# Optimization experiments

Hardware: AMD Instinct MI355X
Metric: run time of the kernel (lower is better)

Reference implementation:

```python
import jax, jax.numpy as jnp
import numpy as np

N, E, IN_DIM, HID, OUT = 50000, 800000, 128, 128, 64


def setup_inputs() -> dict:
    key = jax.random.key(0)
    k = jax.random.split(key, 6)
    h = jax.random.normal(k[0], (N, IN_DIM), dtype=jnp.float32)
    edge_index = jax.random.randint(k[1], (2, E), 0, N, dtype=jnp.int64)
    s_in, s_hid = 1.0 / np.sqrt(IN_DIM), 1.0 / np.sqrt(HID)
    W_gcn = jax.random.uniform(k[2], (IN_DIM, HID), jnp.float32, -s_in, s_in)
    b_gcn = jnp.zeros((HID,), jnp.float32)
    W_fc = jax.random.uniform(k[3], (HID, OUT), jnp.float32, -s_hid, s_hid)
    b_fc = jax.random.uniform(k[4], (OUT,), jnp.float32, -s_hid, s_hid)
    return {"h": h, "edge_index": edge_index, "W_gcn": W_gcn,
            "b_gcn": b_gcn, "W_fc": W_fc, "b_fc": b_fc}


def reference(h, edge_index, W_gcn, b_gcn, W_fc, b_fc):
    n = h.shape[0]
    # GCNConv: transform, add self-loops, symmetric normalization, scatter-add
    x = h @ W_gcn                                   # [N, HID]
    loop = jnp.arange(n, dtype=edge_index.dtype)
    row = jnp.concatenate([edge_index[0], loop])    # source nodes
    col = jnp.concatenate([edge_index[1], loop])    # destination nodes
    deg = jax.ops.segment_sum(jnp.ones_like(col, dtype=x.dtype), col,
                              num_segments=n)       # in-degree incl. self-loop
    dinv = jnp.where(deg > 0, jax.lax.rsqrt(deg), 0.0)
    norm = dinv[row] * dinv[col]                    # [E+N]
    msg = x[row] * norm[:, None]                    # gather + scale
    agg = jax.ops.segment_sum(msg, col, num_segments=n) + b_gcn
    # ReLU then projection
    return jax.nn.relu(agg) @ W_fc + b_fc
```

## Files before the change

kernel.cpp:

```cpp
#include <hip/hip_runtime.h>

#define N_NODES 50000
#define N_EDGES 800000
#define NBKT 196
#define BINB 196
#define CASTB 391
#define BCAP 6144
#define SECAP 1792
#define UTS 136

typedef __attribute__((ext_vector_type(4))) float floatx4;
typedef __attribute__((ext_vector_type(8))) _Float16 half8;
typedef __attribute__((ext_vector_type(4))) _Float16 half4;
typedef __attribute__((ext_vector_type(2))) _Float16 half2v;

#define O_GF    0UL
#define O_DEG   3200UL
#define O_W1    203264UL
#define O_W2    236032UL
#define O_STG   252416UL
#define O_H16   5857792UL

__global__ __launch_bounds__(256) void k_bin(const int* __restrict__ ei,
                                             const float* __restrict__ h,
                                             int* __restrict__ gfill,
                                             unsigned* __restrict__ staging,
                                             const float* __restrict__ Wg,
                                             const float* __restrict__ Wf,
                                             _Float16* __restrict__ W1,
                                             _Float16* __restrict__ W2,
                                             _Float16* __restrict__ h16) {
    int b = blockIdx.x, t = threadIdx.x;
    if (b >= BINB + 96) {
        int wb = b - (BINB + 96);
        int nb = wb * 128;
        int nn = min(128, N_NODES - nb);
        if (nn <= 0) return;
        const floatx4* src = (const floatx4*)(h + (size_t)nb * 128);
        half4* dst = (half4*)(h16 + (size_t)nb * 128);
        int nq = nn * 32;
        for (int i = t; i < nq; i += 256) {
            floatx4 v = src[i];
            half4 o;
            o[0] = (_Float16)v[0]; o[1] = (_Float16)v[1];
            o[2] = (_Float16)v[2]; o[3] = (_Float16)v[3];
            dst[i] = o;
        }
        return;
    }
    if (b >= BINB) {
        int wb = b - BINB;
        if (wb < 64) {
            int i = wb * 256 + t;
            int n = i >> 7, k = i & 127;
            W1[i] = (_Float16)Wg[k * 128 + n];
        } else {
            int i = (wb - 64) * 256 + t;
            int n = i >> 7, k = i & 127;
            W2[i] = (_Float16)Wf[k * 64 + n];
        }
        return;
    }
    __shared__ int cnt[NBKT];
    __shared__ int gbase[NBKT];
    __shared__ int s_i64;
    if (t < 64) {
        unsigned w = ((const unsigned*)ei)[2 * t + 1];
        unsigned long long m = __ballot(w == 0u);
        if (t == 0) s_i64 = (__popcll(m) >= 60) ? 1 : 0;
    }
    for (int i = t; i < NBKT; i += 256) cnt[i] = 0;
    __syncthreads();
    bool i64 = s_i64 != 0;
    int e0 = b * 4096 + t * 16;
    int sv[16], dvv[16];
    if (i64) {
        const int4* ps = (const int4*)(ei) + (e0 >> 1);
        const int4* pd = (const int4*)(ei + 2 * (size_t)N_EDGES) + (e0 >> 1);
#pragma unroll
        for (int g = 0; g < 8; ++g) {
            if (e0 + 2 * g < N_EDGES) {
                int4 s4 = ps[g], d4 = pd[g];
                sv[2 * g] = s4.x; sv[2 * g + 1] = s4.z;
                dvv[2 * g] = d4.x; dvv[2 * g + 1] = d4.z;
            } else { dvv[2 * g] = -1; dvv[2 * g + 1] = -1; }
        }
    } else {
        const int4* ps = (const int4*)(ei) + (e0 >> 2);
        const int4* pd = (const int4*)(ei + (size_t)N_EDGES) + (e0 >> 2);
#pragma unroll
        for (int g = 0; g < 4; ++g) {
            if (e0 + 4 * g < N_EDGES) {
                int4 s4 = ps[g], d4 = pd[g];
                sv[4 * g] = s4.x; sv[4 * g + 1] = s4.y; sv[4 * g + 2] = s4.z; sv[4 * g + 3] = s4.w;
                dvv[4 * g] = d4.x; dvv[4 * g + 1] = d4.y; dvv[4 * g + 2] = d4.z; dvv[4 * g + 3] = d4.w;
            } else { dvv[4 * g] = -1; dvv[4 * g + 1] = -1; dvv[4 * g + 2] = -1; dvv[4 * g + 3] = -1; }
        }
    }
    unsigned pk[16]; int rk[16]; short bk[16];
#pragma unroll
    for (int j = 0; j < 16; ++j) {
        int d = dvv[j];
        if (d >= 0 && e0 + j < N_EDGES) {
            int bkt = d >> 8;
            bk[j] = (short)bkt;
            pk[j] = (unsigned)sv[j] | ((unsigned)(d & 255) << 16);
            rk[j] = atomicAdd(&cnt[bkt], 1);
        } else bk[j] = -1;
    }
    __syncthreads();
    for (int i = t; i < NBKT; i += 256)
        gbase[i] = atomicAdd(&gfill[i], cnt[i]);
    __syncthreads();
#pragma unroll
    for (int j = 0; j < 16; ++j) {
        if (bk[j] >= 0) {
            int pos = gbase[bk[j]] + rk[j];
            if (pos < BCAP) staging[(size_t)bk[j] * BCAP + pos] = pk[j];
        }
    }
}

__global__ __launch_bounds__(256) void k_deg(const int* __restrict__ gfill,
                                             const unsigned* __restrict__ staging,
                                             int* __restrict__ deg_g) {
    __shared__ int deg[256];
    int b = blockIdx.x, t = threadIdx.x;
    int nb = b * 256;
    int nn = min(256, N_NODES - nb);
    if (nn <= 0) return;
    deg[t] = 0;
    __syncthreads();
    int cnt = min(gfill[b], BCAP);
    const unsigned* st = staging + (size_t)b * BCAP;
    for (int i = t; i < cnt; i += 256)
        atomicAdd(&deg[st[i] >> 16], 1);
    __syncthreads();
    if (t < nn) deg_g[nb + t] = deg[t];
}

__global__ __launch_bounds__(256, 8) void k_aggF(const _Float16* __restrict__ h16,
                                                 const int* __restrict__ gfill,
                                                 const unsigned* __restrict__ staging,
                                                 const int* __restrict__ deg_g,
                                                 const _Float16* __restrict__ W1,
                                                 const _Float16* __restrict__ W2,
                                                 const float* __restrict__ bg,
                                                 const float* __restrict__ bfc,
                                                 float* __restrict__ out) {
    __shared__ _Float16 ut[16 * UTS];
    __shared__ _Float16 z[16 * UTS];
    __shared__ unsigned se32[SECAP];
    __shared__ int deg16[16], seg16[16], cur16[16];
    __shared__ float sdv16[16];
    int t = threadIdx.x;
    int wave = t >> 6;
    int lane = t & 63;
    int nb = blockIdx.x * 16;
    int bkt = blockIdx.x >> 4;
    unsigned lo = (unsigned)(blockIdx.x & 15) * 16;
    int cnt = min(gfill[bkt], BCAP);
    if (t < 16) {
        int dg = deg_g[nb + t];
        deg16[t] = dg;
        sdv16[t] = rsqrtf((float)(dg + 1));
    }
    __syncthreads();
    if (t == 0) {
        int s = 0;
#pragma unroll
        for (int k = 0; k < 16; ++k) { seg16[k] = s; cur16[k] = s; s += deg16[k]; }
    }
    __syncthreads();
    const unsigned* st = staging + (size_t)bkt * BCAP;
    for (int i = t; i < cnt; i += 256) {
        unsigned p = st[i];
        unsigned tg = (p >> 16) - lo;
        if (tg < 16u) {
            int rk = atomicAdd(&cur16[tg], 1);
            unsigned src = p & 0xFFFFu;
            unsigned dg = (unsigned)deg_g[src];
            if (rk < SECAP) se32[rk] = (dg << 16) | src;
        }
    }
    __syncthreads();
    for (int q = 0; q < 4; ++q) {
        int tag = wave * 4 + q;
        int node = nb + tag;
        int p0 = seg16[tag];
        int p1 = p0 + deg16[tag];
        float sc = sdv16[tag];
        half2v us = *(const half2v*)(h16 + (size_t)node * 128 + lane * 2);
        float a0 = (float)us[0] * sc, a1 = (float)us[1] * sc;
        for (int base = p0; base < p1; base += 64) {
            int c = p1 - base; if (c > 64) c = 64;
            int idx = 0;
            if (lane < c) idx = (int)se32[base + lane];
            float wf = rsqrtf((float)((unsigned)idx >> 16) + 1.f);
            int j = 0;
            for (; j + 8 <= c; j += 8) {
                int s0 = __shfl(idx, j),     s1 = __shfl(idx, j + 1);
                int s2 = __shfl(idx, j + 2), s3 = __shfl(idx, j + 3);
                int s4 = __shfl(idx, j + 4), s5 = __shfl(idx, j + 5);
                int s6 = __shfl(idx, j + 6), s7 = __shfl(idx, j + 7);
                float f0 = __shfl(wf, j),     f1 = __shfl(wf, j + 1);
                float f2 = __shfl(wf, j + 2), f3 = __shfl(wf, j + 3);
                float f4 = __shfl(wf, j + 4), f5 = __shfl(wf, j + 5);
                float f6 = __shfl(wf, j + 6), f7 = __shfl(wf, j + 7);
                half2v u0 = *(const half2v*)(h16 + (size_t)(s0 & 0xFFFF) * 128 + lane * 2);
                half2v u1 = *(const half2v*)(h16 + (size_t)(s1 & 0xFFFF) * 128 + lane * 2);
                half2v u2 = *(const half2v*)(h16 + (size_t)(s2 & 0xFFFF) * 128 + lane * 2);
                half2v u3 = *(const half2v*)(h16 + (size_t)(s3 & 0xFFFF) * 128 + lane * 2);
                half2v u4 = *(const half2v*)(h16 + (size_t)(s4 & 0xFFFF) * 128 + lane * 2);
                half2v u5 = *(const half2v*)(h16 + (size_t)(s5 & 0xFFFF) * 128 + lane * 2);
                half2v u6 = *(const half2v*)(h16 + (size_t)(s6 & 0xFFFF) * 128 + lane * 2);
                half2v u7 = *(const half2v*)(h16 + (size_t)(s7 & 0xFFFF) * 128 + lane * 2);
                a0 = fmaf((float)u0[0], f0, a0); a1 = fmaf((float)u0[1], f0, a1);
                a0 = fmaf((float)u1[0], f1, a0); a1 = fmaf((float)u1[1], f1, a1);
                a0 = fmaf((float)u2[0], f2, a0); a1 = fmaf((float)u2[1], f2, a1);
                a0 = fmaf((float)u3[0], f3, a0); a1 = fmaf((float)u3[1], f3, a1);
                a0 = fmaf((float)u4[0], f4, a0); a1 = fmaf((float)u4[1], f4, a1);
                a0 = fmaf((float)u5[0], f5, a0); a1 = fmaf((float)u5[1], f5, a1);
                a0 = fmaf((float)u6[0], f6, a0); a1 = fmaf((float)u6[1], f6, a1);
                a0 = fmaf((float)u7[0], f7, a0); a1 = fmaf((float)u7[1], f7, a1);
            }
            for (; j + 4 <= c; j += 4) {
                int s0 = __shfl(idx, j),     s1 = __shfl(idx, j + 1);
                int s2 = __shfl(idx, j + 2), s3 = __shfl(idx, j + 3);
                float f0 = __shfl(wf, j),     f1 = __shfl(wf, j + 1);
                float f2 = __shfl(wf, j + 2), f3 = __shfl(wf, j + 3);
                half2v u0 = *(const half2v*)(h16 + (size_t)(s0 & 0xFFFF) * 128 + lane * 2);
                half2v u1 = *(const half2v*)(h16 + (size_t)(s1 & 0xFFFF) * 128 + lane * 2);
                half2v u2 = *(const half2v*)(h16 + (size_t)(s2 & 0xFFFF) * 128 + lane * 2);
                half2v u3 = *(const half2v*)(h16 + (size_t)(s3 & 0xFFFF) * 128 + lane * 2);
                a0 = fmaf((float)u0[0], f0, a0); a1 = fmaf((float)u0[1], f0, a1);
                a0 = fmaf((float)u1[0], f1, a0); a1 = fmaf((float)u1[1], f1, a1);
                a0 = fmaf((float)u2[0], f2, a0); a1 = fmaf((float)u2[1], f2, a1);
                a0 = fmaf((float)u3[0], f3, a0); a1 = fmaf((float)u3[1], f3, a1);
            }
            for (; j < c; ++j) {
                int s = __shfl(idx, j);
                float f = __shfl(wf, j);
                half2v uu = *(const half2v*)(h16 + (size_t)(s & 0xFFFF) * 128 + lane * 2);
                a0 = fmaf((float)uu[0], f, a0); a1 = fmaf((float)uu[1], f, a1);
            }
        }
        int r = wave * 4 + q;
        ut[r * UTS + lane * 2]     = (_Float16)(a0 * sc);
        ut[r * UTS + lane * 2 + 1] = (_Float16)(a1 * sc);
    }
    __syncthreads();
    int quad = lane >> 4, l15 = lane & 15;
    half8 a[4];
#pragma unroll
    for (int kk = 0; kk < 4; ++kk)
        a[kk] = *(const half8*)(ut + l15 * UTS + kk * 32 + quad * 8);
#pragma unroll
    for (int tt = 0; tt < 2; ++tt) {
        floatx4 acc = {0.f, 0.f, 0.f, 0.f};
        int n = (wave * 2 + tt) * 16 + l15;
#pragma unroll
        for (int kk = 0; kk < 4; ++kk) {
            half8 bb = *(const half8*)(W1 + n * 128 + kk * 32 + quad * 8);
            acc = __builtin_amdgcn_mfma_f32_16x16x32_f16(a[kk], bb, acc, 0, 0, 0);
        }
        float bias = bg[n];
#pragma unroll
        for (int i = 0; i < 4; ++i)
            z[(quad * 4 + i) * UTS + n] = (_Float16)fmaxf(acc[i] + bias, 0.f);
    }
    __syncthreads();
    half8 a2[4];
#pragma unroll
    for (int kk = 0; kk < 4; ++kk)
        a2[kk] = *(const half8*)(z + l15 * UTS + kk * 32 + quad * 8);
    {
        floatx4 acc = {0.f, 0.f, 0.f, 0.f};
        int n = wave * 16 + l15;
#pragma unroll
        for (int kk = 0; kk < 4; ++kk) {
            half8 bb = *(const half8*)(W2 + n * 128 + kk * 32 + quad * 8);
            acc = __builtin_amdgcn_mfma_f32_16x16x32_f16(a2[kk], bb, acc, 0, 0, 0);
        }
        float bias = bfc[n];
#pragma unroll
        for (int i = 0; i < 4; ++i)
            out[(size_t)(nb + quad * 4 + i) * 64 + n] = acc[i] + bias;
    }
}

extern "C" void kernel_launch(void* const* d_in, const int* in_sizes, int n_in,
                              void* d_out, int out_size, void* d_ws, size_t ws_size,
                              hipStream_t stream) {
    (void)in_sizes; (void)n_in; (void)out_size; (void)ws_size;
    const float* h  = (const float*)d_in[0];
    const int*   ei = (const int*)d_in[1];
    const float* Wg = (const float*)d_in[2];
    const float* bg = (const float*)d_in[3];
    const float* Wf = (const float*)d_in[4];
    const float* bf = (const float*)d_in[5];
    float* out = (float*)d_out;

    char* ws = (char*)d_ws;
    int*      gfill = (int*)(ws + O_GF);
    int*      deg_g = (int*)(ws + O_DEG);
    _Float16* W1    = (_Float16*)(ws + O_W1);
    _Float16* W2    = (_Float16*)(ws + O_W2);
    unsigned* staging = (unsigned*)(ws + O_STG);
    _Float16* h16   = (_Float16*)(ws + O_H16);

    hipMemsetAsync(ws, 0, O_W1, stream);
    k_bin<<<BINB + 96 + CASTB, 256, 0, stream>>>(ei, h, gfill, staging,
                                                 Wg, Wf, W1, W2, h16);
    k_deg<<<NBKT, 256, 0, stream>>>(gfill, staging, deg_g);
    k_aggF<<<N_NODES / 16, 256, 0, stream>>>(h16, gfill, staging, deg_g,
                                             W1, W2, bg, bf, out);
}
```

Baseline: 168.4 us.

## Build per-bucket CSR in sort kernel instead of rescanning buckets in aggregation

Replaces the degree-count kernel with a sort kernel that counts per-node degrees, scans them into global CSR row pointers, and scatters 16-bit source ids into a compact edge array. Previously each aggregation block re-read its whole 256-node bucket (about 4K entries) and filtered down to its own 16 nodes, so every bucket was read 16 times. Now each block reads only its contiguous edge slice. The cost is an extra global write and read of the edge array, plus a serial prefix over bucket fills in every sort block. The memset is also narrowed to just the fill counters.

Result: faster. 154.9 us (-8.0%).

```diff
diff --git a/kernel.cpp b/kernel.cpp
--- a/kernel.cpp
+++ b/kernel.cpp
@@ -16,10 +16,12 @@
 
 #define O_GF    0UL
 #define O_DEG   3200UL
-#define O_W1    203264UL
-#define O_W2    236032UL
-#define O_STG   252416UL
-#define O_H16   5857792UL
+#define O_PTR   203264UL
+#define O_W1    403328UL
+#define O_W2    436096UL
+#define O_ESRC  452480UL
+#define O_STG   2052480UL
+#define O_H16   6869376UL
 
 __global__ __launch_bounds__(256) void k_bin(const int* __restrict__ ei,
                                              const float* __restrict__ h,
@@ -121,28 +123,62 @@
     }
 }
 
-__global__ __launch_bounds__(256) void k_deg(const int* __restrict__ gfill,
-                                             const unsigned* __restrict__ staging,
-                                             int* __restrict__ deg_g) {
-    __shared__ int deg[256];
+__global__ __launch_bounds__(256) void k_sort(const unsigned* __restrict__ staging,
+                                              const int* __restrict__ gfill,
+                                              int* __restrict__ ptr,
+                                              int* __restrict__ deg_g,
+                                              unsigned short* __restrict__ esrc) {
+    __shared__ unsigned se[BCAP];
+    __shared__ int lcnt[256];
+    __shared__ int lscan[256];
+    __shared__ int cur[256];
+    __shared__ int s_cb;
     int b = blockIdx.x, t = threadIdx.x;
-    int nb = b * 256;
-    int nn = min(256, N_NODES - nb);
-    if (nn <= 0) return;
-    deg[t] = 0;
-    __syncthreads();
+    int nbase = b * 256;
+    int nn = min(256, N_NODES - nbase);
     int cnt = min(gfill[b], BCAP);
+    if (t < 64) {
+        int acc = 0;
+        for (int i = t; i < b; i += 64) acc += min(gfill[i], BCAP);
+#pragma unroll
+        for (int off = 32; off > 0; off >>= 1) acc += __shfl_down(acc, off);
+        if (t == 0) s_cb = acc;
+    }
+    lcnt[t] = 0;
+    __syncthreads();
+    int cb = s_cb;
     const unsigned* st = staging + (size_t)b * BCAP;
-    for (int i = t; i < cnt; i += 256)
-        atomicAdd(&deg[st[i] >> 16], 1);
-    __syncthreads();
-    if (t < nn) deg_g[nb + t] = deg[t];
+    for (int i = t; i < cnt; i += 256) {
+        unsigned p = st[i];
+        se[i] = p;
+        atomicAdd(&lcnt[p >> 16], 1);
+    }
+    __syncthreads();
+    int v = lcnt[t];
+    lscan[t] = v;
+    __syncthreads();
+    for (int off = 1; off < 256; off <<= 1) {
+        int x = (t >= off) ? lscan[t - off] : 0;
+        __syncthreads(); lscan[t] += x; __syncthreads();
+    }
+    int segstart = cb + (lscan[t] - v);
+    if (t < nn) {
+        ptr[nbase + t] = segstart;
+        deg_g[nbase + t] = v;
+        cur[t] = segstart;
+    }
+    __syncthreads();
+    for (int i = t; i < cnt; i += 256) {
+        unsigned p = se[i];
+        int pos = atomicAdd(&cur[p >> 16], 1);
+        esrc[pos] = (unsigned short)(p & 0xffffu);
+    }
 }
 
 __global__ __launch_bounds__(256, 8) void k_aggF(const _Float16* __restrict__ h16,
-                                                 const int* __restrict__ gfill,
-                                                 const unsigned* __restrict__ staging,
+                                                 const int* __restrict__ ptr,
                                                  const int* __restrict__ deg_g,
+                                                 const unsigned short* __restrict__ esrc,
                                                  const _Float16* __restrict__ W1,
                                                  const _Float16* __restrict__ W2,
                                                  const float* __restrict__ bg,
@@ -151,44 +187,37 @@
     __shared__ _Float16 ut[16 * UTS];
     __shared__ _Float16 z[16 * UTS];
     __shared__ unsigned se32[SECAP];
-    __shared__ int deg16[16], seg16[16], cur16[16];
+    __shared__ int p16[17];
+    __shared__ int deg16[16];
     __shared__ float sdv16[16];
     int t = threadIdx.x;
     int wave = t >> 6;
     int lane = t & 63;
     int nb = blockIdx.x * 16;
-    int bkt = blockIdx.x >> 4;
-    unsigned lo = (unsigned)(blockIdx.x & 15) * 16;
-    int cnt = min(gfill[bkt], BCAP);
     if (t < 16) {
         int dg = deg_g[nb + t];
         deg16[t] = dg;
         sdv16[t] = rsqrtf((float)(dg + 1));
-    }
-    __syncthreads();
-    if (t == 0) {
-        int s = 0;
-#pragma unroll
-        for (int k = 0; k < 16; ++k) { seg16[k] = s; cur16[k] = s; s += deg16[k]; }
-    }
-    __syncthreads();
-    const unsigned* st = staging + (size_t)bkt * BCAP;
-    for (int i = t; i < cnt; i += 256) {
-        unsigned p = st[i];
-        unsigned tg = (p >> 16) - lo;
-        if (tg < 16u) {
-            int rk = atomicAdd(&cur16[tg], 1);
-            unsigned src = p & 0xFFFFu;
-            unsigned dg = (unsigned)deg_g[src];
-            if (rk < SECAP) se32[rk] = (dg << 16) | src;
-        }
+        p16[t] = ptr[nb + t];
+    }
+    __syncthreads();
+    if (t == 0) p16[16] = p16[15] + deg16[15];
+    __syncthreads();
+    int base0 = p16[0];
+    int total = p16[16] - base0;
+    if (total > SECAP) total = SECAP;
+    for (int i = t; i < total; i += 256) {
+        unsigned src = esrc[base0 + i];
+        unsigned dg = (unsigned)deg_g[src];
+        se32[i] = (dg << 16) | src;
     }
     __syncthreads();
     for (int q = 0; q < 4; ++q) {
         int tag = wave * 4 + q;
         int node = nb + tag;
-        int p0 = seg16[tag];
+        int p0 = p16[tag] - base0;
         int p1 = p0 + deg16[tag];
+        if (p1 > SECAP) p1 = SECAP;
         float sc = sdv16[tag];
         half2v us = *(const half2v*)(h16 + (size_t)node * 128 + lane * 2);
         float a0 = (float)us[0] * sc, a1 = (float)us[1] * sc;
@@ -304,15 +333,17 @@
     char* ws = (char*)d_ws;
     int*      gfill = (int*)(ws + O_GF);
     int*      deg_g = (int*)(ws + O_DEG);
+    int*      ptr   = (int*)(ws + O_PTR);
     _Float16* W1    = (_Float16*)(ws + O_W1);
     _Float16* W2    = (_Float16*)(ws + O_W2);
+    unsigned short* esrc = (unsigned short*)(ws + O_ESRC);
     unsigned* staging = (unsigned*)(ws + O_STG);
     _Float16* h16   = (_Float16*)(ws + O_H16);
 
-    hipMemsetAsync(ws, 0, O_W1, stream);
+    hipMemsetAsync(gfill, 0, NBKT * sizeof(int), stream);
     k_bin<<<BINB + 96 + CASTB, 256, 0, stream>>>(ei, h, gfill, staging,
                                                  Wg, Wf, W1, W2, h16);
-    k_deg<<<NBKT, 256, 0, stream>>>(gfill, staging, deg_g);
-    k_aggF<<<N_NODES / 16, 256, 0, stream>>>(h16, gfill, staging, deg_g,
+    k_sort<<<NBKT, 256, 0, stream>>>(staging, gfill, ptr, deg_g, esrc);
+    k_aggF<<<N_NODES / 16, 256, 0, stream>>>(h16, ptr, deg_g, esrc,
                                              W1, W2, bg, bf, out);
 }
```
